# Performance work log

Hardware: AMD Instinct MI355X
Metric: run time of the kernel (lower is better)

## Reference

```python
import jax, jax.numpy as jnp
import numpy as np

N_HEADS = 16
D_K = 64
MAX_LEN = 5000


def setup_inputs() -> dict:
    key = jax.random.key(0)
    ks = jax.random.split(key, 6)
    B, L, D = 4, 1024, 1024
    s = 1.0 / np.sqrt(D).astype(np.float32)
    return {
        "x": jax.random.normal(ks[0], (B, L, D), jnp.float32),
        "W_q": jax.random.normal(ks[1], (D, D), jnp.float32) * s,
        "b_q": jnp.zeros((D,), jnp.float32),
        "W_k": jax.random.normal(ks[2], (D, D), jnp.float32) * s,
        "b_k": jnp.zeros((D,), jnp.float32),
        "W_v": jax.random.normal(ks[3], (D, D), jnp.float32) * s,
        "b_v": jnp.zeros((D,), jnp.float32),
        "W_o": jax.random.normal(ks[4], (D, D), jnp.float32) * s,
        "b_o": jnp.zeros((D,), jnp.float32),
        "Er": jax.random.normal(ks[5], (MAX_LEN, D_K), jnp.float32) * 0.02,
    }


def reference(x, W_q, b_q, W_k, b_k, W_v, b_v, W_o, b_o, Er):
    B, L, D = x.shape
    H = N_HEADS
    dk = D // H
    # torch nn.Linear: y = x @ W.T + b
    Q = (x @ W_q.T + b_q).reshape(B, L, H, dk).transpose(0, 2, 1, 3)  # (B,H,L,dk)
    K = (x @ W_k.T + b_k).reshape(B, L, H, dk).transpose(0, 2, 1, 3)
    V = (x @ W_v.T + b_v).reshape(B, L, H, dk).transpose(0, 2, 1, 3)
    AC = jnp.einsum('bhid,bhjd->bhij', Q, K)  # (B,H,L,L)
    rel_pos = jnp.arange(L - 1, -L, -1) + (MAX_LEN - 1)  # (2L-1,)
    # mode='clip' matches intended math: clamped rows fall in the part that
    # the relative shift slices away.
    Er_embed = jnp.take(Er, rel_pos, axis=0, mode='clip')  # (2L-1, dk)
    BD = jnp.einsum('bhid,rd->bhir', Q, Er_embed)  # (B,H,L,2L-1)
    # _relative_shift: view is a no-op (shape already (B,H,L,2L-1)), then slice
    BD = BD[..., L - 1:]  # (B,H,L,L)
    scores = (AC + BD) / np.sqrt(dk).astype(np.float32)
    attn = jax.nn.softmax(scores, axis=-1)
    out = jnp.einsum('bhij,bhjd->bhid', attn, V)
    out = out.transpose(0, 2, 1, 3).reshape(B, L, D)
    return out @ W_o.T + b_o
```

## Files before the change

### kernel.cpp

```cpp
#include <hip/hip_runtime.h>
#include <cstdint>
#include <cstddef>


typedef __attribute__((ext_vector_type(8))) short short8;
typedef __attribute__((ext_vector_type(4))) float f32x4;

#define MFMA_BF16(a, b, c) __builtin_amdgcn_mfma_f32_16x16x32_bf16((a), (b), (c), 0, 0, 0)

constexpr int kB = 4, kL = 1024, kD = 1024, kH = 16;
constexpr int kBL = kB * kL;
constexpr float kScale = 0.125f * 1.44269504088896340736f;

static __device__ __forceinline__ unsigned short f32_to_bf16(float f) {
  union { float f; uint32_t u; } c; c.f = f;
  uint32_t u = c.u + 0x7fffu + ((c.u >> 16) & 1u);
  return (unsigned short)(u >> 16);
}

static __device__ __forceinline__ uint32_t pack_bf16x2(float a, float b) {
  union { float f; uint32_t u; } ca, cb; ca.f = a; cb.f = b;
  return ((ca.u + 0x8000u) >> 16) | ((cb.u + 0x8000u) & 0xffff0000u);
}

static __device__ __forceinline__ void gload_lds16(const void* g, void* l) {
  __builtin_amdgcn_global_load_lds(
      (const __attribute__((address_space(1))) void*)g,
      (__attribute__((address_space(3))) void*)l, 16, 0, 0);
}

__global__ __launch_bounds__(256)
void cast_all(const float* __restrict__ x,  const float* __restrict__ Wq,
              const float* __restrict__ Wk, const float* __restrict__ Wv,
              const float* __restrict__ Wo,
              unsigned short* __restrict__ xb, unsigned short* __restrict__ Wcat,
              unsigned short* __restrict__ Wob) {
  int i = blockIdx.x * blockDim.x + threadIdx.x;
  const float* src;
  ushort4* dst;
  int off;
  if (i < 1048576) {
    src = x; dst = reinterpret_cast<ushort4*>(xb); off = i;
  } else {
    int j = i - 1048576;
    int seg = j >> 18;
    off = j & 262143;
    if (seg == 0)      { src = Wq; dst = reinterpret_cast<ushort4*>(Wcat); }
    else if (seg == 1) { src = Wk; dst = reinterpret_cast<ushort4*>(Wcat) + 262144; }
    else if (seg == 2) { src = Wv; dst = reinterpret_cast<ushort4*>(Wcat) + 524288; }
    else               { src = Wo; dst = reinterpret_cast<ushort4*>(Wob); }
  }
  float4 v = reinterpret_cast<const float4*>(src)[off];
  ushort4 o;
  o.x = f32_to_bf16(v.x); o.y = f32_to_bf16(v.y);
  o.z = f32_to_bf16(v.z); o.w = f32_to_bf16(v.w);
  dst[off] = o;
}

__global__ __launch_bounds__(256, 2)
void gemm_qkv(const unsigned short* __restrict__ A,
              const unsigned short* __restrict__ Bm,
              const float* __restrict__ bq, const float* __restrict__ bk,
              const float* __restrict__ bv,
              const float* __restrict__ Er,
              unsigned short* __restrict__ Qh, unsigned short* __restrict__ Kh,
              unsigned short* __restrict__ Vth) {
  __shared__ __align__(16) char smem[81920];
  const int tid  = threadIdx.x;
  const int lane = tid & 63, wave = tid >> 6;
  const int quad = lane >> 4, l15 = lane & 15, lhalf = l15 >> 1;
  const int wr = wave >> 1, wc = wave & 1;

  const int bid = blockIdx.x;
  const int xcd = bid & 7, idx = bid >> 3;
  const int m0 = ((xcd >> 1) * 8 + (idx >> 3)) * 128;
  const int n0 = ((xcd & 1) * 8 + (idx & 7)) * 192;

  const int lane_off = (l15 & 1) * 64 + ((quad * 16) ^ ((lhalf & 3) << 4));
  const int aoff = lhalf * 128 + lane_off + wr * 4096;
  const int boff = lhalf * 128 + lane_off + wc * 6144;

  int srowA[2], scolA[2];
#pragma unroll
  for (int j = 0; j < 2; ++j) {
    int poff = (j * 256 + tid) * 16;
    int L = poff ^ (((poff >> 7) & 3) << 4);
    srowA[j] = ((L >> 7) << 1) | ((L >> 6) & 1);
    scolA[j] = (L & 63) >> 1;
  }
  int srowB[3], scolB[3];
#pragma unroll
  for (int j = 0; j < 3; ++j) {
    int poff = (j * 256 + tid) * 16;
    int L = poff ^ (((poff >> 7) & 3) << 4);
    srowB[j] = ((L >> 7) << 1) | ((L >> 6) & 1);
    scolB[j] = (L & 63) >> 1;
  }

  auto stageA = [&](int kh, int tt) {
    char* dst = smem + (tt & 1) * 16384 + kh * 8192 + tid * 16;
    const int kc = tt * 64 + kh * 32;
#pragma unroll
    for (int j = 0; j < 2; ++j)
      gload_lds16(A + (size_t)(m0 + srowA[j]) * 1024 + kc + scolA[j],
                  dst + j * 4096);
  };
  auto stageB = [&](int kh, int tt) {
    char* dst = smem + 32768 + (tt & 1) * 24576 + kh * 12288 + tid * 16;
    const int kc = tt * 64 + kh * 32;
#pragma unroll
    for (int j = 0; j < 3; ++j)
      gload_lds16(Bm + (size_t)(n0 + srowB[j]) * 1024 + kc + scolB[j],
                  dst + j * 4096);
  };

  const f32x4 vzero = {0.f, 0.f, 0.f, 0.f};
  f32x4 acc[4][6];
#pragma unroll
  for (int i = 0; i < 4; ++i)
#pragma unroll
    for (int j = 0; j < 6; ++j) acc[i][j] = vzero;

  stageA(0, 0); stageB(0, 0);
  stageA(1, 0); stageB(1, 0);
  stageA(0, 1); stageB(0, 1);
  asm volatile("s_waitcnt vmcnt(10)" ::: "memory");
  __builtin_amdgcn_s_barrier();

#define LDAB(KH) do {                                                         \
    _Pragma("unroll")                                                         \
    for (int f_ = 0; f_ < 4; ++f_)                                            \
      af[f_] = *(const short8*)(RA + (KH) * 8192 + aoff + f_ * 1024);         \
    _Pragma("unroll")                                                         \
    for (int n_ = 0; n_ < 6; ++n_)                                            \
      bf[n_] = *(const short8*)(RB + (KH) * 12288 + boff + n_ * 1024);        \
  } while (0)
#define BARA() do {                                                           \
    __builtin_amdgcn_s_barrier();                                             \
    asm volatile("s_waitcnt lgkmcnt(0)" ::: "memory");                        \
    __builtin_amdgcn_sched_barrier(0);                                        \
  } while (0)
#define MFMA_24() do {                                                        \
    __builtin_amdgcn_s_setprio(1);                                            \
    _Pragma("unroll")                                                         \
    for (int mq_ = 0; mq_ < 4; ++mq_) {                                       \
      _Pragma("unroll")                                                       \
      for (int nq_ = 0; nq_ < 6; ++nq_)                                       \
        acc[mq_][nq_] = MFMA_BF16(af[mq_], bf[nq_], acc[mq_][nq_]);           \
    }                                                                         \
    __builtin_amdgcn_s_setprio(0);                                            \
  } while (0)

  for (int t = 0; t < 16; ++t) {
    const char* RA = smem + (t & 1) * 16384;
    const char* RB = smem + 32768 + (t & 1) * 24576;
    short8 af[4], bf[6];
    LDAB(0);
    if (t + 1 < 16) { stageA(1, t + 1); stageB(1, t + 1); }
    BARA(); MFMA_24();
    if (t < 15) asm volatile("s_waitcnt vmcnt(10)" ::: "memory");
    else        asm volatile("s_waitcnt vmcnt(0)" ::: "memory");
    __builtin_amdgcn_s_barrier();
    LDAB(1);
    if (t + 2 < 16) { stageA(0, t + 2); stageB(0, t + 2); }
    BARA(); MFMA_24();
    if (t < 14)       asm volatile("s_waitcnt vmcnt(10)" ::: "memory");
    else if (t == 14) asm volatile("s_waitcnt vmcnt(5)" ::: "memory");
    else              asm volatile("s_waitcnt vmcnt(0)" ::: "memory");
    __builtin_amdgcn_s_barrier();
  }

#undef LDAB
#undef BARA
#undef MFMA_24

  const int gmb = m0 + wr * 64;
  const int bb  = gmb >> 10, i0l = gmb & 1023;
  unsigned short* Wv = (unsigned short*)smem + (size_t)wave * 2048;

#pragma unroll
  for (int nf = 0; nf < 6; ++nf) {
    const int n    = n0 + wc * 96 + nf * 16;
    const int wsel = n >> 10;
    const int nin  = n & 1023;
    const int hh   = nin >> 6, d0 = nin & 63;
    const size_t bh = (size_t)(bb * 16 + hh);

    if (wsel == 0) {
#pragma unroll
      for (int mf = 0; mf < 4; ++mf)
#pragma unroll
        for (int r = 0; r < 4; ++r) {
          const int i = i0l + mf * 16 + quad * 4 + r;
          float v = (acc[mf][nf][r] + bq[nin + l15]) * kScale;
          Qh[(bh * 1024 + i) * 64 + d0 + l15] = f32_to_bf16(v);
        }
    } else if (wsel == 1) {
#pragma unroll
      for (int mf = 0; mf < 4; ++mf)
#pragma unroll
        for (int r = 0; r < 4; ++r) {
          const int i = i0l + mf * 16 + quad * 4 + r;
          float v = acc[mf][nf][r] + bk[nin + l15] +
                    Er[(size_t)(4999 - i) * 64 + d0 + l15];
          Kh[(bh * 1024 + i) * 64 + d0 + l15] = f32_to_bf16(v);
        }
    } else {
#pragma unroll
      for (int mf = 0; mf < 4; ++mf) {
        ushort4 pk;
        pk.x = f32_to_bf16(acc[mf][nf][0] + bv[nin + l15]);
        pk.y = f32_to_bf16(acc[mf][nf][1] + bv[nin + l15]);
        pk.z = f32_to_bf16(acc[mf][nf][2] + bv[nin + l15]);
        pk.w = f32_to_bf16(acc[mf][nf][3] + bv[nin + l15]);
        *(ushort4*)&Wv[(size_t)l15 * 64 + mf * 16 + quad * 4] = pk;
      }
#pragma unroll
      for (int p = 0; p < 2; ++p) {
        const int u = p * 64 + lane;
        const int dl = u >> 3, ch = (u & 7) * 8;
        short8 vv = *(const short8*)&Wv[(size_t)dl * 64 + ch];
        *(short8*)&Vth[(bh * 64 + d0 + dl) * 1024 + i0l + ch] = vv;
      }
    }
  }
}

__global__ __launch_bounds__(256)
void gemm_out(const unsigned short* __restrict__ A,
              const unsigned short* __restrict__ Bm,
              const float* __restrict__ bias,
              float* __restrict__ outf) {
  __shared__ __align__(16) char smem[49152];
  const int tid  = threadIdx.x;
  const int lane = tid & 63, wave = tid >> 6;
  const int quad = lane >> 4, l15 = lane & 15;
  const int m0 = blockIdx.y * 128, n0 = blockIdx.x * 64;

  const int afo = (l15 >> 1) * 128 + (l15 & 1) * 64 +
                  ((quad * 16) ^ (((l15 >> 1) & 3) << 4));

  int arow[4], acol[4], akh[4];
#pragma unroll
  for (int j = 0; j < 4; ++j) {
    int u = j * 256 + tid;
    akh[j] = u >> 9;
    int poff = (u & 511) * 16;
    int L = poff ^ (((poff >> 7) & 3) << 4);
    arow[j] = ((L >> 7) << 1) | ((L >> 6) & 1);
    acol[j] = (L & 63) >> 1;
  }
  int brow[2], bcol[2], bkh[2];
#pragma unroll
  for (int j = 0; j < 2; ++j) {
    int u = j * 256 + tid;
    bkh[j] = u >> 8;
    int poff = (u & 255) * 16;
    int L = poff ^ (((poff >> 7) & 3) << 4);
    brow[j] = ((L >> 7) << 1) | ((L >> 6) & 1);
    bcol[j] = (L & 63) >> 1;
  }

  auto stageG = [&](int buf, int t) {
    char* base = smem + buf * 24576;
    const int kc = t * 64;
#pragma unroll
    for (int j = 0; j < 4; ++j) {
      int u = j * 256 + tid;
      gload_lds16(A + (size_t)(m0 + arow[j]) * 1024 + kc + akh[j] * 32 + acol[j],
                  base + u * 16);
    }
#pragma unroll
    for (int j = 0; j < 2; ++j) {
      int u = j * 256 + tid;
      gload_lds16(Bm + (size_t)(n0 + brow[j]) * 1024 + kc + bkh[j] * 32 + bcol[j],
                  base + 16384 + u * 16);
    }
  };

  const f32x4 vzero = {0.f, 0.f, 0.f, 0.f};
  f32x4 acc[2][4];
#pragma unroll
  for (int i = 0; i < 2; ++i)
#pragma unroll
    for (int j = 0; j < 4; ++j) acc[i][j] = vzero;

  stageG(0, 0);
  for (int t = 0; t < 16; ++t) {
    const int cur = t & 1;
    if (t < 15) stageG(cur ^ 1, t + 1);
    if (t < 15) asm volatile("s_waitcnt vmcnt(6)" ::: "memory");
    else        asm volatile("s_waitcnt vmcnt(0)" ::: "memory");
    __builtin_amdgcn_s_barrier();
    __builtin_amdgcn_sched_barrier(0);
    const char* Ab = smem + cur * 24576;
    const char* Bb = Ab + 16384;
#pragma unroll
    for (int ks = 0; ks < 2; ++ks) {
      short8 af[2], bfv[4];
#pragma unroll
      for (int mt = 0; mt < 2; ++mt)
        af[mt] = *(const short8*)(Ab + ks * 8192 + wave * 2048 + mt * 1024 + afo);
#pragma unroll
      for (int nt = 0; nt < 4; ++nt)
        bfv[nt] = *(const short8*)(Bb + ks * 4096 + nt * 1024 + afo);
#pragma unroll
      for (int mt = 0; mt < 2; ++mt)
#pragma unroll
        for (int nt = 0; nt < 4; ++nt)
          acc[mt][nt] = MFMA_BF16(af[mt], bfv[nt], acc[mt][nt]);
    }
    __builtin_amdgcn_s_barrier();
    __builtin_amdgcn_sched_barrier(0);
  }

#pragma unroll
  for (int mt = 0; mt < 2; ++mt)
#pragma unroll
    for (int nt = 0; nt < 4; ++nt)
#pragma unroll
      for (int r = 0; r < 4; ++r) {
        const int gm = m0 + wave * 32 + mt * 16 + quad * 4 + r;
        const int gn = n0 + nt * 16 + l15;
        outf[(size_t)gm * 1024 + gn] = acc[mt][nt][r] + bias[gn];
      }
}

__global__ __launch_bounds__(256)
void attn_kernel(const unsigned short* __restrict__ Q,
                 const unsigned short* __restrict__ Kp,
                 const unsigned short* __restrict__ Vt,
                 unsigned short* __restrict__ Ao) {
  __shared__ unsigned short Ks[2][2][64 * 32];
  __shared__ unsigned short Vs[2][2][64 * 32];
  __shared__ unsigned short Plds[4][32 * 72];
  const int tid  = threadIdx.x;
  const int lane = tid & 63, wave = tid >> 6;
  const int quad = lane >> 4, l15 = lane & 15;
  const int bh = blockIdx.x;
  const int qb = blockIdx.y;
  const size_t base  = (size_t)bh * (kL * 64);
  const size_t vbase = (size_t)bh * (64 * kL);
  const int i0 = qb * 128 + wave * 32;

  short8 qf[2][2];
#pragma unroll
  for (int mt = 0; mt < 2; ++mt)
#pragma unroll
    for (int ks = 0; ks < 2; ++ks)
      qf[mt][ks] = *(const short8*)
          &Q[base + (size_t)(i0 + mt * 16 + l15) * 64 + ks * 32 + quad * 8];

  auto stage = [&](int buf, int kb) {
#pragma unroll
    for (int j = 0; j < 2; ++j) {
      int u = j * 256 + tid;
      int half = u >> 8, row = (u >> 2) & 63, c = (u & 3) * 8;
      gload_lds16(Kp + base + (size_t)(kb * 64 + row) * 64 + half * 32 + c,
                  (char*)&Ks[buf][0][0] + (size_t)u * 16);
      gload_lds16(Vt + vbase + (size_t)row * kL + kb * 64 + half * 32 + c,
                  (char*)&Vs[buf][0][0] + (size_t)u * 16);
    }
  };

  const f32x4 vzero = {0.f, 0.f, 0.f, 0.f};
  f32x4 of[2][4];
#pragma unroll
  for (int mt = 0; mt < 2; ++mt)
#pragma unroll
    for (int dt = 0; dt < 4; ++dt) of[mt][dt] = vzero;
  float lsum[2] = {0.f, 0.f};

  unsigned short* Pw = Plds[wave];

  stage(0, 0);
  __syncthreads();

  for (int kb = 0; kb < 16; ++kb) {
    const int cur = kb & 1, nxt = cur ^ 1;
    if (kb < 15) stage(nxt, kb + 1);

    short8 kf[4][2];
#pragma unroll
    for (int nt = 0; nt < 4; ++nt)
#pragma unroll
      for (int ks = 0; ks < 2; ++ks)
        kf[nt][ks] = *(const short8*)&Ks[cur][ks][(nt * 16 + l15) * 32 + quad * 8];
    f32x4 sf[2][4];
#pragma unroll
    for (int mt = 0; mt < 2; ++mt)
#pragma unroll
      for (int nt = 0; nt < 4; ++nt) {
        sf[mt][nt] = MFMA_BF16(kf[nt][0], qf[mt][0], vzero);
        sf[mt][nt] = MFMA_BF16(kf[nt][1], qf[mt][1], sf[mt][nt]);
      }

#pragma unroll
    for (int mt = 0; mt < 2; ++mt)
#pragma unroll
      for (int nt = 0; nt < 4; ++nt) {
        float p0 = __builtin_amdgcn_exp2f(sf[mt][nt][0]);
        float p1 = __builtin_amdgcn_exp2f(sf[mt][nt][1]);
        float p2 = __builtin_amdgcn_exp2f(sf[mt][nt][2]);
        float p3 = __builtin_amdgcn_exp2f(sf[mt][nt][3]);
        lsum[mt] += (p0 + p1) + (p2 + p3);
        uint2 w;
        w.x = pack_bf16x2(p0, p1);
        w.y = pack_bf16x2(p2, p3);
        *(uint2*)&Pw[(mt * 16 + l15) * 72 + nt * 16 + quad * 4] = w;
      }
    short8 pf[2][2];
#pragma unroll
    for (int mt = 0; mt < 2; ++mt)
#pragma unroll
      for (int ks = 0; ks < 2; ++ks)
        pf[mt][ks] = *(const short8*)&Pw[(mt * 16 + l15) * 72 + ks * 32 + quad * 8];

    short8 vf[4][2];
#pragma unroll
    for (int dt = 0; dt < 4; ++dt)
#pragma unroll
      for (int ks = 0; ks < 2; ++ks)
        vf[dt][ks] = *(const short8*)&Vs[cur][ks][(dt * 16 + l15) * 32 + quad * 8];
#pragma unroll
    for (int mt = 0; mt < 2; ++mt)
#pragma unroll
      for (int dt = 0; dt < 4; ++dt) {
        of[mt][dt] = MFMA_BF16(pf[mt][0], vf[dt][0], of[mt][dt]);
        of[mt][dt] = MFMA_BF16(pf[mt][1], vf[dt][1], of[mt][dt]);
      }

    __syncthreads();
  }

  float rl[2][4];
#pragma unroll
  for (int mt = 0; mt < 2; ++mt) {
    float s = lsum[mt];
    s += __shfl_xor(s, 16);
    s += __shfl_xor(s, 32);
#pragma unroll
    for (int r = 0; r < 4; ++r)
      rl[mt][r] = __builtin_amdgcn_rcpf(__shfl(s, quad * 4 + r));
  }

  const int b = bh >> 4, h = bh & 15;
#pragma unroll
  for (int mt = 0; mt < 2; ++mt)
#pragma unroll
    for (int dt = 0; dt < 4; ++dt)
#pragma unroll
      for (int r = 0; r < 4; ++r) {
        const int ig = i0 + mt * 16 + quad * 4 + r;
        float v = of[mt][dt][r] * rl[mt][r];
        Ao[((size_t)(b * 1024 + ig)) * 1024 + h * 64 + dt * 16 + l15] = f32_to_bf16(v);
      }
}

extern "C" void kernel_launch(void* const* d_in, const int* in_sizes, int n_in,
                              void* d_out, int out_size, void* d_ws, size_t ws_size,
                              hipStream_t stream) {
  const float* x   = (const float*)d_in[0];
  const float* W_q = (const float*)d_in[1];
  const float* b_q = (const float*)d_in[2];
  const float* W_k = (const float*)d_in[3];
  const float* b_k = (const float*)d_in[4];
  const float* W_v = (const float*)d_in[5];
  const float* b_v = (const float*)d_in[6];
  const float* W_o = (const float*)d_in[7];
  const float* b_o = (const float*)d_in[8];
  const float* Er  = (const float*)d_in[9];
  float* out = (float*)d_out;

  char* ws = (char*)d_ws;
  unsigned short* xb   = (unsigned short*)(ws + (size_t)0);
  unsigned short* Wcat = (unsigned short*)(ws + ((size_t)8  << 20));
  unsigned short* Wob  = (unsigned short*)(ws + ((size_t)14 << 20));
  unsigned short* Qh   = (unsigned short*)(ws + ((size_t)16 << 20));
  unsigned short* Kh   = (unsigned short*)(ws + ((size_t)24 << 20));
  unsigned short* Vth  = (unsigned short*)(ws + ((size_t)32 << 20));
  unsigned short* Aoh  = (unsigned short*)(ws + ((size_t)40 << 20));

  cast_all<<<8192, 256, 0, stream>>>(x, W_q, W_k, W_v, W_o, xb, Wcat, Wob);

  gemm_qkv<<<512, 256, 0, stream>>>(
      xb, Wcat, b_q, b_k, b_v, Er, Qh, Kh, Vth);

  attn_kernel<<<dim3(kB * kH, kL / 128), 256, 0, stream>>>(Qh, Kh, Vth, Aoh);

  gemm_out<<<dim3(16, 32), 256, 0, stream>>>(Aoh, Wob, b_o, out);
}
```

Measured before the change: 172.9 us.

## Shrink QKV GEMM tile to 128x128 with single-buffered LDS for higher occupancy

The QKV projection GEMM moves from 128x192 tiles with double-buffered, software-pipelined LDS staging to 128x128 tiles with a single 32KB buffer and plain syncthreads around each k-step. The grid grows from 512 to 768 blocks and launch bounds now target 3 blocks per CU, so more waves can hide latency. The cost is that global loads no longer overlap with MFMA work inside a block, and each block reuses fewer B columns. The epilogue is restructured so each wave handles one full 64-wide head slice, which simplifies the V transpose.

```diff
diff --git a/kernel.cpp b/kernel.cpp
--- a/kernel.cpp
+++ b/kernel.cpp
@@ -57,7 +57,7 @@
   dst[off] = o;
 }
 
-__global__ __launch_bounds__(256, 2)
+__global__ __launch_bounds__(256, 3)
 void gemm_qkv(const unsigned short* __restrict__ A,
               const unsigned short* __restrict__ Bm,
               const float* __restrict__ bq, const float* __restrict__ bk,
@@ -65,7 +65,7 @@
               const float* __restrict__ Er,
               unsigned short* __restrict__ Qh, unsigned short* __restrict__ Kh,
               unsigned short* __restrict__ Vth) {
-  __shared__ __align__(16) char smem[81920];
+  __shared__ __align__(16) char smem[32768];
   const int tid  = threadIdx.x;
   const int lane = tid & 63, wave = tid >> 6;
   const int quad = lane >> 4, l15 = lane & 15, lhalf = l15 >> 1;
@@ -73,129 +73,95 @@
 
   const int bid = blockIdx.x;
   const int xcd = bid & 7, idx = bid >> 3;
-  const int m0 = ((xcd >> 1) * 8 + (idx >> 3)) * 128;
-  const int n0 = ((xcd & 1) * 8 + (idx & 7)) * 192;
+  const int mi = idx / 12, ni = idx - mi * 12;
+  const int m0 = ((xcd >> 1) * 8 + mi) * 128;
+  const int n0 = ((xcd & 1) * 12 + ni) * 128;
 
   const int lane_off = (l15 & 1) * 64 + ((quad * 16) ^ ((lhalf & 3) << 4));
   const int aoff = lhalf * 128 + lane_off + wr * 4096;
-  const int boff = lhalf * 128 + lane_off + wc * 6144;
-
-  int srowA[2], scolA[2];
+  const int boff = lhalf * 128 + lane_off + wc * 4096;
+
+  int srow[2], scol[2];
 #pragma unroll
   for (int j = 0; j < 2; ++j) {
     int poff = (j * 256 + tid) * 16;
     int L = poff ^ (((poff >> 7) & 3) << 4);
-    srowA[j] = ((L >> 7) << 1) | ((L >> 6) & 1);
-    scolA[j] = (L & 63) >> 1;
-  }
-  int srowB[3], scolB[3];
-#pragma unroll
-  for (int j = 0; j < 3; ++j) {
-    int poff = (j * 256 + tid) * 16;
-    int L = poff ^ (((poff >> 7) & 3) << 4);
-    srowB[j] = ((L >> 7) << 1) | ((L >> 6) & 1);
-    scolB[j] = (L & 63) >> 1;
+    srow[j] = ((L >> 7) << 1) | ((L >> 6) & 1);
+    scol[j] = (L & 63) >> 1;
   }
 
   auto stageA = [&](int kh, int tt) {
-    char* dst = smem + (tt & 1) * 16384 + kh * 8192 + tid * 16;
+    char* dst = smem + kh * 8192 + tid * 16;
     const int kc = tt * 64 + kh * 32;
 #pragma unroll
     for (int j = 0; j < 2; ++j)
-      gload_lds16(A + (size_t)(m0 + srowA[j]) * 1024 + kc + scolA[j],
+      gload_lds16(A + (size_t)(m0 + srow[j]) * 1024 + kc + scol[j],
                   dst + j * 4096);
   };
   auto stageB = [&](int kh, int tt) {
-    char* dst = smem + 32768 + (tt & 1) * 24576 + kh * 12288 + tid * 16;
+    char* dst = smem + 16384 + kh * 8192 + tid * 16;
     const int kc = tt * 64 + kh * 32;
 #pragma unroll
-    for (int j = 0; j < 3; ++j)
-      gload_lds16(Bm + (size_t)(n0 + srowB[j]) * 1024 + kc + scolB[j],
+    for (int j = 0; j < 2; ++j)
+      gload_lds16(Bm + (size_t)(n0 + srow[j]) * 1024 + kc + scol[j],
                   dst + j * 4096);
   };
 
   const f32x4 vzero = {0.f, 0.f, 0.f, 0.f};
-  f32x4 acc[4][6];
+  f32x4 acc[4][4];
 #pragma unroll
   for (int i = 0; i < 4; ++i)
 #pragma unroll
-    for (int j = 0; j < 6; ++j) acc[i][j] = vzero;
-
-  stageA(0, 0); stageB(0, 0);
-  stageA(1, 0); stageB(1, 0);
-  stageA(0, 1); stageB(0, 1);
-  asm volatile("s_waitcnt vmcnt(10)" ::: "memory");
-  __builtin_amdgcn_s_barrier();
-
-#define LDAB(KH) do {                                                         \
-    _Pragma("unroll")                                                         \
-    for (int f_ = 0; f_ < 4; ++f_)                                            \
-      af[f_] = *(const short8*)(RA + (KH) * 8192 + aoff + f_ * 1024);         \
-    _Pragma("unroll")                                                         \
-    for (int n_ = 0; n_ < 6; ++n_)                                            \
-      bf[n_] = *(const short8*)(RB + (KH) * 12288 + boff + n_ * 1024);        \
-  } while (0)
-#define BARA() do {                                                           \
-    __builtin_amdgcn_s_barrier();                                             \
-    asm volatile("s_waitcnt lgkmcnt(0)" ::: "memory");                        \
-    __builtin_amdgcn_sched_barrier(0);                                        \
-  } while (0)
-#define MFMA_24() do {                                                        \
-    __builtin_amdgcn_s_setprio(1);                                            \
-    _Pragma("unroll")                                                         \
-    for (int mq_ = 0; mq_ < 4; ++mq_) {                                       \
-      _Pragma("unroll")                                                       \
-      for (int nq_ = 0; nq_ < 6; ++nq_)                                       \
-        acc[mq_][nq_] = MFMA_BF16(af[mq_], bf[nq_], acc[mq_][nq_]);           \
-    }                                                                         \
-    __builtin_amdgcn_s_setprio(0);                                            \
-  } while (0)
+    for (int j = 0; j < 4; ++j) acc[i][j] = vzero;
 
   for (int t = 0; t < 16; ++t) {
-    const char* RA = smem + (t & 1) * 16384;
-    const char* RB = smem + 32768 + (t & 1) * 24576;
-    short8 af[4], bf[6];
-    LDAB(0);
-    if (t + 1 < 16) { stageA(1, t + 1); stageB(1, t + 1); }
-    BARA(); MFMA_24();
-    if (t < 15) asm volatile("s_waitcnt vmcnt(10)" ::: "memory");
-    else        asm volatile("s_waitcnt vmcnt(0)" ::: "memory");
-    __builtin_amdgcn_s_barrier();
-    LDAB(1);
-    if (t + 2 < 16) { stageA(0, t + 2); stageB(0, t + 2); }
-    BARA(); MFMA_24();
-    if (t < 14)       asm volatile("s_waitcnt vmcnt(10)" ::: "memory");
-    else if (t == 14) asm volatile("s_waitcnt vmcnt(5)" ::: "memory");
-    else              asm volatile("s_waitcnt vmcnt(0)" ::: "memory");
-    __builtin_amdgcn_s_barrier();
-  }
-
-#undef LDAB
-#undef BARA
-#undef MFMA_24
-
-  const int gmb = m0 + wr * 64;
-  const int bb  = gmb >> 10, i0l = gmb & 1023;
-  unsigned short* Wv = (unsigned short*)smem + (size_t)wave * 2048;
-
-#pragma unroll
-  for (int nf = 0; nf < 6; ++nf) {
-    const int n    = n0 + wc * 96 + nf * 16;
-    const int wsel = n >> 10;
-    const int nin  = n & 1023;
-    const int hh   = nin >> 6, d0 = nin & 63;
-    const size_t bh = (size_t)(bb * 16 + hh);
-
-    if (wsel == 0) {
+    __syncthreads();
+    stageA(0, t); stageA(1, t); stageB(0, t); stageB(1, t);
+    __syncthreads();
+#pragma unroll
+    for (int ks = 0; ks < 2; ++ks) {
+      short8 af[4], bf[4];
+#pragma unroll
+      for (int mf = 0; mf < 4; ++mf)
+        af[mf] = *(const short8*)(smem + ks * 8192 + aoff + mf * 1024);
+#pragma unroll
+      for (int nf = 0; nf < 4; ++nf)
+        bf[nf] = *(const short8*)(smem + 16384 + ks * 8192 + boff + nf * 1024);
+#pragma unroll
+      for (int mf = 0; mf < 4; ++mf)
+#pragma unroll
+        for (int nf = 0; nf < 4; ++nf)
+          acc[mf][nf] = MFMA_BF16(af[mf], bf[nf], acc[mf][nf]);
+    }
+  }
+  __syncthreads();
+
+  const int gmb  = m0 + wr * 64;
+  const int bb   = gmb >> 10, i0l = gmb & 1023;
+  const int nb   = n0 + wc * 64;
+  const int wsel = nb >> 10;
+  const int nin0 = nb & 1023;
+  const int hh   = nin0 >> 6;
+  const size_t bh = (size_t)(bb * 16 + hh);
+
+  if (wsel == 0) {
+#pragma unroll
+    for (int nf = 0; nf < 4; ++nf) {
+      const int nin = nin0 + nf * 16;
 #pragma unroll
       for (int mf = 0; mf < 4; ++mf)
 #pragma unroll
         for (int r = 0; r < 4; ++r) {
           const int i = i0l + mf * 16 + quad * 4 + r;
           float v = (acc[mf][nf][r] + bq[nin + l15]) * kScale;
-          Qh[(bh * 1024 + i) * 64 + d0 + l15] = f32_to_bf16(v);
+          Qh[(bh * 1024 + i) * 64 + (nin & 63) + l15] = f32_to_bf16(v);
         }
-    } else if (wsel == 1) {
+    }
+  } else if (wsel == 1) {
+#pragma unroll
+    for (int nf = 0; nf < 4; ++nf) {
+      const int nin = nin0 + nf * 16;
+      const int d0  = nin & 63;
 #pragma unroll
       for (int mf = 0; mf < 4; ++mf)
 #pragma unroll
@@ -205,7 +171,12 @@
                     Er[(size_t)(4999 - i) * 64 + d0 + l15];
           Kh[(bh * 1024 + i) * 64 + d0 + l15] = f32_to_bf16(v);
         }
-    } else {
+    }
+  } else {
+    unsigned short* W = (unsigned short*)smem + (size_t)wave * 4096;
+#pragma unroll
+    for (int nf = 0; nf < 4; ++nf) {
+      const int nin = nin0 + nf * 16;
 #pragma unroll
       for (int mf = 0; mf < 4; ++mf) {
         ushort4 pk;
@@ -213,15 +184,15 @@
         pk.y = f32_to_bf16(acc[mf][nf][1] + bv[nin + l15]);
         pk.z = f32_to_bf16(acc[mf][nf][2] + bv[nin + l15]);
         pk.w = f32_to_bf16(acc[mf][nf][3] + bv[nin + l15]);
-        *(ushort4*)&Wv[(size_t)l15 * 64 + mf * 16 + quad * 4] = pk;
-      }
-#pragma unroll
-      for (int p = 0; p < 2; ++p) {
-        const int u = p * 64 + lane;
-        const int dl = u >> 3, ch = (u & 7) * 8;
-        short8 vv = *(const short8*)&Wv[(size_t)dl * 64 + ch];
-        *(short8*)&Vth[(bh * 64 + d0 + dl) * 1024 + i0l + ch] = vv;
-      }
+        *(ushort4*)&W[(size_t)(nf * 16 + l15) * 64 + mf * 16 + quad * 4] = pk;
+      }
+    }
+#pragma unroll
+    for (int p = 0; p < 8; ++p) {
+      const int u = p * 64 + lane;
+      const int d = u >> 3, ch = (u & 7) * 8;
+      short8 vv = *(const short8*)&W[(size_t)d * 64 + ch];
+      *(short8*)&Vth[(bh * 64 + d) * 1024 + i0l + ch] = vv;
     }
   }
 }
@@ -483,7 +454,7 @@
 
   cast_all<<<8192, 256, 0, stream>>>(x, W_q, W_k, W_v, W_o, xb, Wcat, Wob);
 
-  gemm_qkv<<<512, 256, 0, stream>>>(
+  gemm_qkv<<<768, 256, 0, stream>>>(
       xb, Wcat, b_q, b_k, b_v, Er, Qh, Kh, Vth);
 
   attn_kernel<<<dim3(kB * kH, kL / 128), 256, 0, stream>>>(Qh, Kh, Vth, Aoh);
```

Measured after the change: 174.1 us. About the same (+0.7%).
